# Kernel tuning notes

Measured on AMD Instinct MI355X. Metric: run time of the kernel, lower is better.

## Reference

```python
import jax, jax.numpy as jnp
import numpy as np

N, IN_FEATS, HIDDEN, N_CLASSES = 12000, 256, 256, 40
EPS = 1e-12  # F.normalize default eps


def setup_inputs() -> dict:
    key = jax.random.key(0)
    ks = jax.random.split(key, 6)
    # dense adjacency, scaled like a row-normalized graph operator
    adj = jax.random.uniform(ks[0], (N, N), jnp.float32) * (1.0 / 64.0)
    x = jax.random.normal(ks[1], (N, IN_FEATS), jnp.float32)
    # xavier-uniform-like weights, zero biases (matches init_params)
    def xavier(k, fan_in, fan_out):
        lim = np.sqrt(6.0 / (fan_in + fan_out)).astype(np.float32)
        return jax.random.uniform(k, (fan_in, fan_out), jnp.float32, -lim, lim)
    W0 = xavier(ks[2], IN_FEATS, HIDDEN)
    W1 = xavier(ks[3], HIDDEN, HIDDEN)
    W2 = xavier(ks[4], HIDDEN, N_CLASSES)
    b0 = jnp.zeros((HIDDEN,), jnp.float32)
    b1 = jnp.zeros((HIDDEN,), jnp.float32)
    b2 = jnp.zeros((N_CLASSES,), jnp.float32)
    return {"adj": adj, "x": x, "W0": W0, "b0": b0, "W1": W1, "b1": b1, "W2": W2, "b2": b2}


def _l2_normalize(h):
    # F.normalize(h): rows divided by max(||row||_2, eps)
    norm = jnp.sqrt(jnp.sum(h * h, axis=1, keepdims=True))
    return h / jnp.maximum(norm, EPS)


def reference(adj, x, W0, b0, W1, b1, W2, b2):
    # layer 0: aggregate -> linear -> bias -> relu -> l2-normalize (dropout=eval identity)
    h = _l2_normalize(jax.nn.relu((adj @ x) @ W0 + b0))
    # layer 1 (hidden)
    h = _l2_normalize(jax.nn.relu((adj @ h) @ W1 + b1))
    # output layer: no activation / normalize / dropout
    h = (adj @ h) @ W2 + b2
    return h
```

## Files before the change

kernel.cpp:

```cpp
#include <hip/hip_runtime.h>
#include <hip/hip_bf16.h>

#define M_ROWS 12000
#define K_PAD  12032
#define FEAT   256
#define NCLS   40
#define NSLICE 5
#define NTILES 188
#define NBM    47
#define PSLABE (M_ROWS * FEAT)
#define TILE_SHORTS 16384
#define HALF_SHORTS 8192
#define ITILE 16384
#define IHALF 8192

typedef __attribute__((ext_vector_type(4))) float f32x4;
typedef __attribute__((ext_vector_type(8))) short s16x8;
typedef __attribute__((ext_vector_type(4))) short s16x4;
typedef __attribute__((ext_vector_type(4))) int   i32x4;
typedef __attribute__((ext_vector_type(2))) int   i32x2;
typedef unsigned int u32;

__device__ __forceinline__ short f2bf(float f){
  __hip_bfloat16 h = __float2bfloat16(f);
  union { __hip_bfloat16 h; short s; } u; u.h = h; return u.s;
}
__device__ __forceinline__ float bf2f(short s){
  union { float f; u32 u; } v; v.u = ((u32)(unsigned short)s) << 16; return v.f;
}

__device__ __forceinline__ f32x4 mfma16(s16x8 a, s16x8 b, f32x4 c){
  return __builtin_amdgcn_mfma_f32_16x16x32_bf16(a, b, c, 0, 0, 0);
}

__device__ __forceinline__ void gl16(const void* g, void* l){
  __builtin_amdgcn_global_load_lds(
      (const __attribute__((address_space(1))) u32*)g,
      (__attribute__((address_space(3))) u32*)l, 16, 0, 0);
}

#define VM6   do { asm volatile("s_waitcnt vmcnt(6)" ::: "memory"); \
                   __builtin_amdgcn_sched_barrier(0); } while(0)
#define VM4   do { asm volatile("s_waitcnt vmcnt(4)" ::: "memory"); \
                   __builtin_amdgcn_sched_barrier(0); } while(0)
#define VM2   do { asm volatile("s_waitcnt vmcnt(2)" ::: "memory"); \
                   __builtin_amdgcn_sched_barrier(0); } while(0)
#define VM0   do { asm volatile("s_waitcnt vmcnt(0)" ::: "memory"); \
                   __builtin_amdgcn_sched_barrier(0); } while(0)
#define LGK0  do { asm volatile("s_waitcnt lgkmcnt(0)" ::: "memory"); \
                   __builtin_amdgcn_sched_barrier(0); } while(0)
#define BARR  do { __builtin_amdgcn_s_barrier(); \
                   __builtin_amdgcn_sched_barrier(0); } while(0)

__device__ __forceinline__ int swz(int r){ return (r & 3) ^ ((r >> 2) & 3); }

__device__ __forceinline__ int q8(float v, float s){ return (int)(v * s + 0.5f); }

__global__ __launch_bounds__(256) void k_transpose_pack(const float* __restrict__ src,
                                                        short* __restrict__ Bpack){
  const int t = threadIdx.x;
  if (blockIdx.x == 375){
    short* d = Bpack + (size_t)187 * TILE_SHORTS + HALF_SHORTS + t * 32;
    s16x8 z = (s16x8)0;
    #pragma unroll
    for (int i = 0; i < 4; ++i) *(s16x8*)(d + 8*i) = z;
    return;
  }
  __shared__ float tile[32][257];
  const int r0 = blockIdx.x * 32;
  {
    const int r = t >> 3, cs = (t & 7) * 32;
    const float* s = src + (size_t)(r0 + r) * FEAT + cs;
    #pragma unroll
    for (int i = 0; i < 8; ++i){
      f32x4 v = *(const f32x4*)(s + 4*i);
      tile[r][cs + 4*i + 0] = v[0];
      tile[r][cs + 4*i + 1] = v[1];
      tile[r][cs + 4*i + 2] = v[2];
      tile[r][cs + 4*i + 3] = v[3];
    }
  }
  __syncthreads();
  const int c = t;
  const int kt = r0 >> 6, hh = (r0 >> 5) & 1, sc = swz(c);
  short* d = Bpack + (size_t)kt * TILE_SHORTS + hh * HALF_SHORTS + c * 32;
  #pragma unroll
  for (int i = 0; i < 4; ++i){
    s16x8 o;
    #pragma unroll
    for (int j = 0; j < 8; ++j) o[j] = f2bf(tile[8*i + j][c]);
    *(s16x8*)(d + ((i ^ sc) * 8)) = o;
  }
}

__global__ __launch_bounds__(256) void k_zpad(char* __restrict__ Bpk8){
  const int t = threadIdx.x;
  i32x4 z = {0,0,0,0};
  *(i32x4*)(Bpk8 + (size_t)187 * ITILE + IHALF + t * 16) = z;
  *(i32x4*)(Bpk8 + (size_t)187 * ITILE + IHALF + 4096 + t * 16) = z;
}

__global__ __launch_bounds__(512, 2) void k_gemm_l0(const float* __restrict__ adj,
                                                    const short* __restrict__ Bpack,
                                                    char* __restrict__ Apk8,
                                                    short* __restrict__ Pbase){
  __shared__ __align__(16) short lds[2][4][8192];

  const int t = threadIdx.x;
  const int w = t >> 6, l = t & 63;
  const int wm = w >> 2, wn = w & 3;
  const int lr = l & 15, lg = l >> 4;

  int id = blockIdx.x;
  {
    const int xcd = id & 7, idx = id >> 3;
    id = (xcd < 3 ? xcd * 30 : 90 + (xcd - 3) * 29) + idx;
  }
  const int bm = id % NBM, s = id / NBM;
  const int row0 = bm * 256;
  const int u0  = (s < 3) ? s * 38 : 114 + (s - 3) * 37;
  const int nst = (s < 3) ? 38 : 37;

  const char* Bb = (const char*)Bpack;
  const size_t tp = (size_t)t * 16;
  char* Aw = Apk8 + (size_t)bm * NTILES * ITILE;

  size_t abase[2];
  #pragma unroll
  for (int p = 0; p < 2; ++p){
    const int si = p * 512 + t;
    const int r  = si >> 2, sl = si & 3;
    int grow = row0 + r; if (grow > M_ROWS - 1) grow = M_ROWS - 1;
    abase[p] = (size_t)grow * M_ROWS + (size_t)((sl ^ swz(r)) * 8);
  }

  f32x4 av0[4], av1[4];

#define ISSUE_A0(kt) do{ \
    av0[0] = *(const f32x4*)(adj + abase[0] + (kt)*64);      \
    av0[1] = *(const f32x4*)(adj + abase[0] + (kt)*64 + 4);  \
    av0[2] = *(const f32x4*)(adj + abase[1] + (kt)*64);      \
    av0[3] = *(const f32x4*)(adj + abase[1] + (kt)*64 + 4); }while(0)
#define ISSUE_A1(kt) do{ \
    av1[0] = *(const f32x4*)(adj + abase[0] + (kt)*64 + 32);     \
    av1[1] = *(const f32x4*)(adj + abase[0] + (kt)*64 + 32 + 4); \
    av1[2] = *(const f32x4*)(adj + abase[1] + (kt)*64 + 32);     \
    av1[3] = *(const f32x4*)(adj + abase[1] + (kt)*64 + 32 + 4); }while(0)

#define CVT_WRITE_A(q, h, kt, AV) do{                                         \
    _Pragma("unroll")                                                         \
    for (int p = 0; p < 2; ++p){                                              \
      s16x8 o;                                                                \
      _Pragma("unroll")                                                       \
      for (int j = 0; j < 4; ++j){ o[j] = f2bf(AV[2*p][j]); o[4+j] = f2bf(AV[2*p+1][j]); } \
      const int si = p * 512 + t;                                             \
      *(s16x8*)&lds[q][h][si * 8] = o;                                        \
      int w0_ = 0, w1_ = 0;                                                   \
      _Pragma("unroll")                                                       \
      for (int j = 0; j < 4; ++j){                                            \
        w0_ |= (q8(AV[2*p][j],   8128.0f) & 255) << (8*j);                    \
        w1_ |= (q8(AV[2*p+1][j], 8128.0f) & 255) << (8*j);                    \
      }                                                                       \
      i32x2 pk_; pk_[0] = w0_; pk_[1] = w1_;                                  \
      *(i32x2*)(Aw + (size_t)(kt) * ITILE + (h) * IHALF + si * 8) = pk_;      \
    } }while(0)

#define ST_BH(q, h, kt) do{                                                   \
    const char* s_ = Bb + (size_t)(kt) * 32768 + (h) * 16384 + tp;            \
    gl16(s_,        (char*)&lds[q][2+(h)][0] + w*1024);                       \
    gl16(s_ + 8192, (char*)&lds[q][2+(h)][0] + 8192 + w*1024); }while(0)

#define AF(q, h, mf) \
    (*(const s16x8*)&lds[q][h][ (wm*128 + (mf)*16 + lr) * 32 + \
      ((lg ^ swz(wm*128 + (mf)*16 + lr)) * 8) ])
#define BF(q, h, nf) \
    (*(const s16x8*)&lds[q][2+(h)][ (wn*64 + (nf)*16 + lr) * 32 + \
      ((lg ^ swz(wn*64 + (nf)*16 + lr)) * 8) ])

  f32x4 acc[8][4];
  #pragma unroll
  for (int m = 0; m < 8; ++m)
    #pragma unroll
    for (int n = 0; n < 4; ++n) acc[m][n] = (f32x4)(0.0f);

  ISSUE_A0(u0); ST_BH(0, 0, u0);
  ISSUE_A1(u0); ST_BH(0, 1, u0);
  VM6;  CVT_WRITE_A(0, 0, u0, av0);
  VM4;  CVT_WRITE_A(0, 1, u0, av1);
  LGK0;
  BARR;

  for (int t2 = 0; t2 < nst; ++t2){
    const int q = t2 & 1, qn = q ^ 1;
    const bool stg = (t2 + 1 < nst);
    const int ktn = u0 + t2 + 1;

    s16x8 bfr[4], af[4];

    #pragma unroll
    for (int n = 0; n < 4; ++n) bfr[n] = BF(q, 0, n);
    #pragma unroll
    for (int m = 0; m < 4; ++m) af[m] = AF(q, 0, m);
    if (stg){ ISSUE_A0(ktn); ST_BH(qn, 0, ktn); }
    BARR;
    __builtin_amdgcn_s_setprio(1);
    #pragma unroll
    for (int m = 0; m < 4; ++m)
      #pragma unroll
      for (int n = 0; n < 4; ++n)
        acc[m][n] = mfma16(af[m], bfr[n], acc[m][n]);
    __builtin_amdgcn_s_setprio(0);
    BARR;

    #pragma unroll
    for (int m = 0; m < 4; ++m) af[m] = AF(q, 0, m + 4);
    if (stg){ ISSUE_A1(ktn); ST_BH(qn, 1, ktn); }
    BARR;
    __builtin_amdgcn_s_setprio(1);
    #pragma unroll
    for (int m = 0; m < 4; ++m)
      #pragma unroll
      for (int n = 0; n < 4; ++n)
        acc[m + 4][n] = mfma16(af[m], bfr[n], acc[m + 4][n]);
    __builtin_amdgcn_s_setprio(0);
    BARR;

    if (stg) { VM6; } else { VM4; }
    #pragma unroll
    for (int n = 0; n < 4; ++n) bfr[n] = BF(q, 1, n);
    #pragma unroll
    for (int m = 0; m < 4; ++m) af[m] = AF(q, 1, m);
    if (stg){ CVT_WRITE_A(qn, 0, ktn, av0); }
    BARR;
    __builtin_amdgcn_s_setprio(1);
    #pragma unroll
    for (int m = 0; m < 4; ++m)
      #pragma unroll
      for (int n = 0; n < 4; ++n)
        acc[m][n] = mfma16(af[m], bfr[n], acc[m][n]);
    __builtin_amdgcn_s_setprio(0);
    BARR;

    #pragma unroll
    for (int m = 0; m < 4; ++m) af[m] = AF(q, 1, m + 4);
    if (stg){ VM4; CVT_WRITE_A(qn, 1, ktn, av1); }
    BARR;
    __builtin_amdgcn_s_setprio(1);
    #pragma unroll
    for (int m = 0; m < 4; ++m)
      #pragma unroll
      for (int n = 0; n < 4; ++n)
        acc[m + 4][n] = mfma16(af[m], bfr[n], acc[m + 4][n]);
    __builtin_amdgcn_s_setprio(0);
    if (stg) LGK0;
    BARR;
  }
#undef ISSUE_A0
#undef ISSUE_A1
#undef CVT_WRITE_A
#undef ST_BH
#undef AF
#undef BF

  short* P = Pbase + (size_t)s * PSLABE;
  #pragma unroll
  for (int m = 0; m < 8; ++m){
    const int row = row0 + wm*128 + m*16 + lg*4;
    #pragma unroll
    for (int n = 0; n < 4; ++n){
      const int col = wn*64 + n*16 + lr;
      short* pp = P + (size_t)row * FEAT + col;
      #pragma unroll
      for (int r = 0; r < 4; ++r)
        if (row + r < M_ROWS) pp[(size_t)r * FEAT] = f2bf(acc[m][n][r]);
    }
  }
}

__global__ __launch_bounds__(512, 2) void k_gemm8i(const char* __restrict__ Apk8,
                                                   const char* __restrict__ Bpk8,
                                                   short* __restrict__ Pbase){
  __shared__ __align__(16) char lds8[2][4][8192];

  const int t = threadIdx.x;
  const int w = t >> 6, l = t & 63;
  const int wm = w >> 2, wn = w & 3;
  const int lr = l & 15, lg = l >> 4;

  int id = blockIdx.x;
  {
    const int xcd = id & 7, idx = id >> 3;
    id = (xcd < 3 ? xcd * 30 : 90 + (xcd - 3) * 29) + idx;
  }
  const int bm = id % NBM, s = id / NBM;
  const int row0 = bm * 256;
  const int u0  = (s < 3) ? s * 38 : 114 + (s - 3) * 37;
  const int nst = (s < 3) ? 38 : 37;

  const char* Ab = Apk8 + (size_t)bm * NTILES * ITILE;
  const char* Bb = Bpk8;
  const size_t tp = (size_t)t * 16;

#define ST_AH(q, h, kt) \
    gl16(Ab + (size_t)(kt) * ITILE + (h) * IHALF + tp, (char*)&lds8[q][h][0] + w*1024)
#define ST_BH(q, h, kt) \
    gl16(Bb + (size_t)(kt) * ITILE + (h) * IHALF + tp, (char*)&lds8[q][2+(h)][0] + w*1024)

#define AF8(q, h, mf) \
    (*(const long*)&lds8[q][h][ (wm*128 + (mf)*16 + lr) * 32 + \
      ((lg ^ swz(wm*128 + (mf)*16 + lr)) * 8) ])
#define BF8(q, h, nf) \
    (*(const long*)&lds8[q][2+(h)][ (wn*64 + (nf)*16 + lr) * 32 + \
      ((lg ^ swz(wn*64 + (nf)*16 + lr)) * 8) ])

  i32x4 acc[8][4];
  #pragma unroll
  for (int m = 0; m < 8; ++m)
    #pragma unroll
    for (int n = 0; n < 4; ++n) acc[m][n] = (i32x4){0,0,0,0};

  ST_BH(0, 0, u0); ST_AH(0, 0, u0);
  ST_BH(0, 1, u0); ST_AH(0, 1, u0);
  VM2;
  BARR;

  for (int t2 = 0; t2 < nst; ++t2){
    const int q = t2 & 1, qn = q ^ 1;
    const bool stg = (t2 + 1 < nst);
    const int ktn = u0 + t2 + 1;

    long bfr[4], af[4];

    #pragma unroll
    for (int n = 0; n < 4; ++n) bfr[n] = BF8(q, 0, n);
    #pragma unroll
    for (int m = 0; m < 4; ++m) af[m] = AF8(q, 0, m);
    if (stg) ST_BH(qn, 0, ktn);
    BARR;
    __builtin_amdgcn_s_setprio(1);
    #pragma unroll
    for (int m = 0; m < 4; ++m)
      #pragma unroll
      for (int n = 0; n < 4; ++n)
        acc[m][n] = __builtin_amdgcn_mfma_i32_16x16x32_i8(af[m], bfr[n], acc[m][n], 0, 0, 0);
    __builtin_amdgcn_s_setprio(0);
    BARR;

    #pragma unroll
    for (int m = 0; m < 4; ++m) af[m] = AF8(q, 0, m + 4);
    if (stg) ST_AH(qn, 0, ktn);
    BARR;
    __builtin_amdgcn_s_setprio(1);
    #pragma unroll
    for (int m = 0; m < 4; ++m)
      #pragma unroll
      for (int n = 0; n < 4; ++n)
        acc[m + 4][n] = __builtin_amdgcn_mfma_i32_16x16x32_i8(af[m], bfr[n], acc[m + 4][n], 0, 0, 0);
    __builtin_amdgcn_s_setprio(0);
    if (stg) { VM2; } else { VM0; }
    BARR;

    #pragma unroll
    for (int n = 0; n < 4; ++n) bfr[n] = BF8(q, 1, n);
    #pragma unroll
    for (int m = 0; m < 4; ++m) af[m] = AF8(q, 1, m);
    if (stg) ST_BH(qn, 1, ktn);
    BARR;
    __builtin_amdgcn_s_setprio(1);
    #pragma unroll
    for (int m = 0; m < 4; ++m)
      #pragma unroll
      for (int n = 0; n < 4; ++n)
        acc[m][n] = __builtin_amdgcn_mfma_i32_16x16x32_i8(af[m], bfr[n], acc[m][n], 0, 0, 0);
    __builtin_amdgcn_s_setprio(0);
    BARR;

    #pragma unroll
    for (int m = 0; m < 4; ++m) af[m] = AF8(q, 1, m + 4);
    if (stg) ST_AH(qn, 1, ktn);
    BARR;
    __builtin_amdgcn_s_setprio(1);
    #pragma unroll
    for (int m = 0; m < 4; ++m)
      #pragma unroll
      for (int n = 0; n < 4; ++n)
        acc[m + 4][n] = __builtin_amdgcn_mfma_i32_16x16x32_i8(af[m], bfr[n], acc[m + 4][n], 0, 0, 0);
    __builtin_amdgcn_s_setprio(0);
    if (stg) { VM2; }
    BARR;
  }
#undef ST_AH
#undef ST_BH
#undef AF8
#undef BF8

  const float ds = 1.0f / 1032256.0f;
  short* P = Pbase + (size_t)s * PSLABE;
  #pragma unroll
  for (int m = 0; m < 8; ++m){
    const int row = row0 + wm*128 + m*16 + lg*4;
    #pragma unroll
    for (int n = 0; n < 4; ++n){
      const int col = wn*64 + n*16 + lr;
      short* pp = P + (size_t)row * FEAT + col;
      #pragma unroll
      for (int r = 0; r < 4; ++r)
        if (row + r < M_ROWS) pp[(size_t)r * FEAT] = f2bf((float)acc[m][n][r] * ds);
    }
  }
}

__global__ __launch_bounds__(256) void k_fused2(const short* __restrict__ Pb,
                                                const float* __restrict__ W,
                                                const float* __restrict__ b,
                                                char* __restrict__ Bpk8){
  __shared__ float ylds[32][257];
  __shared__ float red[32][33];
  __shared__ float scale[32];
  const int t  = threadIdx.x;
  const int r0 = blockIdx.x * 32;
  {
    const int r = t >> 3, cs = (t & 7) * 32;
    const size_t off = (size_t)(r0 + r) * FEAT + cs;
    float aa[32];
    {
      const short* p0 = Pb + off;
      #pragma unroll
      for (int i4 = 0; i4 < 4; ++i4){
        s16x8 v = *(const s16x8*)(p0 + i4*8);
        #pragma unroll
        for (int e = 0; e < 8; ++e) aa[i4*8 + e] = bf2f(v[e]);
      }
    }
    #pragma unroll
    for (int s = 1; s < NSLICE; ++s){
      const short* ps = Pb + (size_t)s * PSLABE + off;
      #pragma unroll
      for (int i4 = 0; i4 < 4; ++i4){
        s16x8 v = *(const s16x8*)(ps + i4*8);
        #pragma unroll
        for (int e = 0; e < 8; ++e) aa[i4*8 + e] += bf2f(v[e]);
      }
    }
    #pragma unroll
    for (int k = 0; k < 32; ++k) ylds[r][cs + k] = aa[k];
  }
  __syncthreads();

  const int rg = t >> 5;
  const int cg = t & 31;
  float acc[4][8];
  {
    float bias[8];
    #pragma unroll
    for (int j = 0; j < 8; ++j) bias[j] = b[cg*8 + j];
    #pragma unroll
    for (int i = 0; i < 4; ++i)
      #pragma unroll
      for (int j = 0; j < 8; ++j) acc[i][j] = bias[j];
  }

  #pragma unroll 4
  for (int k = 0; k < FEAT; ++k){
    float yv[4];
    #pragma unroll
    for (int i = 0; i < 4; ++i) yv[i] = ylds[rg*4 + i][k];
    f32x4 w0 = *(const f32x4*)(W + (size_t)k * FEAT + cg*8);
    f32x4 w1 = *(const f32x4*)(W + (size_t)k * FEAT + cg*8 + 4);
    #pragma unroll
    for (int i = 0; i < 4; ++i){
      #pragma unroll
      for (int j = 0; j < 4; ++j){
        acc[i][j]     += yv[i] * w0[j];
        acc[i][4 + j] += yv[i] * w1[j];
      }
    }
  }

  #pragma unroll
  for (int i = 0; i < 4; ++i){
    float ss = 0.0f;
    #pragma unroll
    for (int j = 0; j < 8; ++j){
      float v = fmaxf(acc[i][j], 0.0f);
      acc[i][j] = v;
      ss += v * v;
    }
    red[rg*4 + i][cg] = ss;
  }
  __syncthreads();
  if (t < 32){
    float ssum = 0.0f;
    #pragma unroll
    for (int j = 0; j < 32; ++j) ssum += red[t][j];
    scale[t] = 1.0f / fmaxf(sqrtf(ssum), 1e-12f);
  }
  __syncthreads();

  float sc[4];
  float dith[4];
  #pragma unroll
  for (int i = 0; i < 4; ++i){
    sc[i] = scale[rg*4 + i];
    const int k = r0 + rg*4 + i;
    float x = (float)k * 0.6180339887f;
    dith[i] = x - floorf(x);
  }

  const int kb = r0 + rg * 4;
  const int kt = kb >> 6, hh = (kb >> 5) & 1, g = (kb >> 3) & 3, e0 = kb & 7;
  char* dbase = Bpk8 + (size_t)kt * ITILE + hh * IHALF;
  #pragma unroll
  for (int j = 0; j < 8; ++j){
    const int c = cg * 8 + j;
    int pk = 0;
    #pragma unroll
    for (int i = 0; i < 4; ++i){
      int q = (int)(acc[i][j] * sc[i] * 127.0f + dith[i]);
      pk |= (q & 255) << (8*i);
    }
    *(int*)(dbase + c * 32 + ((g ^ swz(c)) * 8) + e0) = pk;
  }
}

__global__ __launch_bounds__(256) void k_final2(const short* __restrict__ Pb,
                                                const float* __restrict__ W2,
                                                const float* __restrict__ b2,
                                                float* __restrict__ out){
  __shared__ float ylds[32][257];
  const int t  = threadIdx.x;
  const int r0 = blockIdx.x * 32;
  {
    const int r = t >> 3, cs = (t & 7) * 32;
    const size_t off = (size_t)(r0 + r) * FEAT + cs;
    float aa[32];
    {
      const short* p0 = Pb + off;
      #pragma unroll
      for (int i4 = 0; i4 < 4; ++i4){
        s16x8 v = *(const s16x8*)(p0 + i4*8);
        #pragma unroll
        for (int e = 0; e < 8; ++e) aa[i4*8 + e] = bf2f(v[e]);
      }
    }
    #pragma unroll
    for (int s = 1; s < NSLICE; ++s){
      const short* ps = Pb + (size_t)s * PSLABE + off;
      #pragma unroll
      for (int i4 = 0; i4 < 4; ++i4){
        s16x8 v = *(const s16x8*)(ps + i4*8);
        #pragma unroll
        for (int e = 0; e < 8; ++e) aa[i4*8 + e] += bf2f(v[e]);
      }
    }
    #pragma unroll
    for (int k = 0; k < 32; ++k) ylds[r][cs + k] = aa[k];
  }
  __syncthreads();

  #pragma unroll
  for (int e = t; e < 32 * NCLS; e += 256){
    const int r = e / NCLS, n = e % NCLS;
    float a = b2[n];
    #pragma unroll 8
    for (int k = 0; k < FEAT; ++k)
      a = fmaf(ylds[r][k], W2[(size_t)k * NCLS + n], a);
    out[(size_t)(r0 + r) * NCLS + n] = a;
  }
}

extern "C" void kernel_launch(void* const* d_in, const int* in_sizes, int n_in,
                              void* d_out, int out_size, void* d_ws, size_t ws_size,
                              hipStream_t stream){
  const float* adj = (const float*)d_in[0];
  const float* x   = (const float*)d_in[1];
  const float* W0  = (const float*)d_in[2];
  const float* b0  = (const float*)d_in[3];
  const float* W1  = (const float*)d_in[4];
  const float* b1  = (const float*)d_in[5];
  const float* W2  = (const float*)d_in[6];
  const float* b2  = (const float*)d_in[7];
  float* out = (float*)d_out;

  char* ws = (char*)d_ws;
  const size_t BPACK_BYTES = (size_t)NTILES * TILE_SHORTS * 2;
  const size_t BPK8_BYTES  = (size_t)NTILES * ITILE;
  const size_t APK8_BYTES  = (size_t)NBM * NTILES * ITILE;

  short* Bpack = (short*)ws;
  char*  Bpk8  = ws + BPACK_BYTES;
  char*  Apk8  = ws + BPACK_BYTES + BPK8_BYTES;
  short* P     = (short*)(ws + BPACK_BYTES + BPK8_BYTES + APK8_BYTES);

  const dim3 b256(256), b512(512);

  k_transpose_pack<<<376, b256, 0, stream>>>(x, Bpack);
  k_zpad<<<1, b256, 0, stream>>>(Bpk8);

  k_gemm_l0<<<NBM * NSLICE, b512, 0, stream>>>(adj, Bpack, Apk8, P);
  k_fused2<<<375, b256, 0, stream>>>(P, W0, b0, Bpk8);
  k_gemm8i<<<NBM * NSLICE, b512, 0, stream>>>(Apk8, Bpk8, P);
  k_fused2<<<375, b256, 0, stream>>>(P, W1, b1, Bpk8);
  k_gemm8i<<<NBM * NSLICE, b512, 0, stream>>>(Apk8, Bpk8, P);
  k_final2<<<375, b256, 0, stream>>>(P, W2, b2, out);
}
```

Before: 433.5 us.

## Split adjacency int8 quantization into a separate pass; layer-0 GEMM reads int8

```diff
diff --git a/kernel.cpp b/kernel.cpp
--- a/kernel.cpp
+++ b/kernel.cpp
@@ -18,7 +18,6 @@
 typedef __attribute__((ext_vector_type(8))) short s16x8;
 typedef __attribute__((ext_vector_type(4))) short s16x4;
 typedef __attribute__((ext_vector_type(4))) int   i32x4;
-typedef __attribute__((ext_vector_type(2))) int   i32x2;
 typedef unsigned int u32;
 
 __device__ __forceinline__ short f2bf(float f){
@@ -39,10 +38,6 @@
       (__attribute__((address_space(3))) u32*)l, 16, 0, 0);
 }
 
-#define VM6   do { asm volatile("s_waitcnt vmcnt(6)" ::: "memory"); \
-                   __builtin_amdgcn_sched_barrier(0); } while(0)
-#define VM4   do { asm volatile("s_waitcnt vmcnt(4)" ::: "memory"); \
-                   __builtin_amdgcn_sched_barrier(0); } while(0)
 #define VM2   do { asm volatile("s_waitcnt vmcnt(2)" ::: "memory"); \
                    __builtin_amdgcn_sched_barrier(0); } while(0)
 #define VM0   do { asm volatile("s_waitcnt vmcnt(0)" ::: "memory"); \
@@ -100,11 +95,57 @@
   *(i32x4*)(Bpk8 + (size_t)187 * ITILE + IHALF + 4096 + t * 16) = z;
 }
 
-__global__ __launch_bounds__(512, 2) void k_gemm_l0(const float* __restrict__ adj,
-                                                    const short* __restrict__ Bpack,
-                                                    char* __restrict__ Apk8,
-                                                    short* __restrict__ Pbase){
-  __shared__ __align__(16) short lds[2][4][8192];
+__global__ __launch_bounds__(512) void k_conv8(const float* __restrict__ adj,
+                                               char* __restrict__ Apk8){
+  __shared__ char stg[8][12352];
+  const int t  = threadIdx.x;
+  const int rb = blockIdx.x * 8;
+  const int bm = rb >> 8;
+  const int rbase_loc = rb & 255;
+
+  for (int r = 0; r < 8; ++r){
+    const int R = rb + r;
+    const float* rowp = adj + (size_t)(R < M_ROWS ? R : 0) * M_ROWS;
+    #pragma unroll
+    for (int ch = 0; ch < 6; ++ch){
+      const int c0 = ch * 2048 + t * 4;
+      f32x4 v = (f32x4)(0.0f);
+      if (R < M_ROWS && c0 < M_ROWS) v = *(const f32x4*)(rowp + c0);
+      int pk = 0;
+      #pragma unroll
+      for (int j = 0; j < 4; ++j) pk |= (q8(v[j], 8128.0f) & 255) << (8*j);
+      *(int*)&stg[r][c0] = pk;
+    }
+  }
+  __syncthreads();
+
+  char* out = Apk8 + (size_t)bm * NTILES * ITILE;
+  #pragma unroll
+  for (int it = 0; it < 12; ++it){
+    const int tau = t + it * 512;
+    if (tau < 6016){
+      const int p = tau >> 4, c = tau & 15;
+      const int tl = p >> 1, h = p & 1;
+      const int r = c >> 1, sl2 = (c & 1) * 2;
+      const int rloc = rbase_loc + r;
+      const int sw = swz(rloc);
+      const int colb = tl * 64 + h * 32;
+      long lo = *(const long*)&stg[r][colb + ((sl2     ^ sw) * 8)];
+      long hi = *(const long*)&stg[r][colb + (((sl2+1) ^ sw) * 8)];
+      i32x4 o;
+      o[0] = (int)lo; o[1] = (int)(lo >> 32);
+      o[2] = (int)hi; o[3] = (int)(hi >> 32);
+      *(i32x4*)(out + (size_t)tl * ITILE + h * IHALF + rloc * 32 + sl2 * 8) = o;
+    }
+  }
+}
+
+__global__ __launch_bounds__(512, 2) void k_gemm_l0b(const char* __restrict__ Apk8,
+                                                     const short* __restrict__ Bpack,
+                                                     short* __restrict__ Pbase){
+  __shared__ __align__(16) short Abf[2][2][8192];
+  __shared__ __align__(16) short Bl [2][2][8192];
+  __shared__ __align__(16) char  Ai8[16384];
 
   const int t = threadIdx.x;
   const int w = t >> 6, l = t & 63;
@@ -121,60 +162,40 @@
   const int u0  = (s < 3) ? s * 38 : 114 + (s - 3) * 37;
   const int nst = (s < 3) ? 38 : 37;
 
-  const char* Bb = (const char*)Bpack;
+  const char* Ab8 = Apk8 + (size_t)bm * NTILES * ITILE;
+  const char* Bb  = (const char*)Bpack;
   const size_t tp = (size_t)t * 16;
-  char* Aw = Apk8 + (size_t)bm * NTILES * ITILE;
-
-  size_t abase[2];
-  #pragma unroll
-  for (int p = 0; p < 2; ++p){
-    const int si = p * 512 + t;
-    const int r  = si >> 2, sl = si & 3;
-    int grow = row0 + r; if (grow > M_ROWS - 1) grow = M_ROWS - 1;
-    abase[p] = (size_t)grow * M_ROWS + (size_t)((sl ^ swz(r)) * 8);
-  }
-
-  f32x4 av0[4], av1[4];
-
-#define ISSUE_A0(kt) do{ \
-    av0[0] = *(const f32x4*)(adj + abase[0] + (kt)*64);      \
-    av0[1] = *(const f32x4*)(adj + abase[0] + (kt)*64 + 4);  \
-    av0[2] = *(const f32x4*)(adj + abase[1] + (kt)*64);      \
-    av0[3] = *(const f32x4*)(adj + abase[1] + (kt)*64 + 4); }while(0)
-#define ISSUE_A1(kt) do{ \
-    av1[0] = *(const f32x4*)(adj + abase[0] + (kt)*64 + 32);     \
-    av1[1] = *(const f32x4*)(adj + abase[0] + (kt)*64 + 32 + 4); \
-    av1[2] = *(const f32x4*)(adj + abase[1] + (kt)*64 + 32);     \
-    av1[3] = *(const f32x4*)(adj + abase[1] + (kt)*64 + 32 + 4); }while(0)
-
-#define CVT_WRITE_A(q, h, kt, AV) do{                                         \
+
+#define ST_B(q, h, kt) do{                                                    \
+    const char* s_ = Bb + (size_t)(kt) * 32768 + (h) * 16384 + tp;            \
+    gl16(s_,        (char*)&Bl[q][h][0] + w*1024);                            \
+    gl16(s_ + 8192, (char*)&Bl[q][h][0] + 8192 + w*1024); }while(0)
+#define ST_AI(kt) do{                                                         \
+    gl16(Ab8 + (size_t)(kt) * ITILE + tp,        (char*)Ai8 + w*1024);        \
+    gl16(Ab8 + (size_t)(kt) * ITILE + 8192 + tp, (char*)Ai8 + 8192 + w*1024); }while(0)
+
+#define CONV_A(qn) do{                                                        \
+    const int h_ = t >> 8;                                                    \
+    const int ti = (t & 255) * 32;                                            \
+    const char* sp = &Ai8[h_*8192 + ti];                                      \
+    short* dp = &Abf[qn][h_][ti];                                             \
     _Pragma("unroll")                                                         \
-    for (int p = 0; p < 2; ++p){                                              \
+    for (int j = 0; j < 4; ++j){                                              \
+      long v = *(const long*)(sp + j*8);                                      \
       s16x8 o;                                                                \
       _Pragma("unroll")                                                       \
-      for (int j = 0; j < 4; ++j){ o[j] = f2bf(AV[2*p][j]); o[4+j] = f2bf(AV[2*p+1][j]); } \
-      const int si = p * 512 + t;                                             \
-      *(s16x8*)&lds[q][h][si * 8] = o;                                        \
-      int w0_ = 0, w1_ = 0;                                                   \
-      _Pragma("unroll")                                                       \
-      for (int j = 0; j < 4; ++j){                                            \
-        w0_ |= (q8(AV[2*p][j],   8128.0f) & 255) << (8*j);                    \
-        w1_ |= (q8(AV[2*p+1][j], 8128.0f) & 255) << (8*j);                    \
+      for (int e = 0; e < 8; ++e){                                            \
+        int b_ = (int)((unsigned long)(v >> (8*e)) & 255);                    \
+        o[e] = f2bf((float)b_ * (1.0f/8128.0f));                              \
       }                                                                       \
-      i32x2 pk_; pk_[0] = w0_; pk_[1] = w1_;                                  \
-      *(i32x2*)(Aw + (size_t)(kt) * ITILE + (h) * IHALF + si * 8) = pk_;      \
+      *(s16x8*)(dp + j*8) = o;                                                \
     } }while(0)
 
-#define ST_BH(q, h, kt) do{                                                   \
-    const char* s_ = Bb + (size_t)(kt) * 32768 + (h) * 16384 + tp;            \
-    gl16(s_,        (char*)&lds[q][2+(h)][0] + w*1024);                       \
-    gl16(s_ + 8192, (char*)&lds[q][2+(h)][0] + 8192 + w*1024); }while(0)
-
-#define AF(q, h, mf) \
-    (*(const s16x8*)&lds[q][h][ (wm*128 + (mf)*16 + lr) * 32 + \
+#define AFb(q, h, mf) \
+    (*(const s16x8*)&Abf[q][h][ (wm*128 + (mf)*16 + lr) * 32 + \
       ((lg ^ swz(wm*128 + (mf)*16 + lr)) * 8) ])
-#define BF(q, h, nf) \
-    (*(const s16x8*)&lds[q][2+(h)][ (wn*64 + (nf)*16 + lr) * 32 + \
+#define BFb(q, h, nf) \
+    (*(const s16x8*)&Bl[q][h][ (wn*64 + (nf)*16 + lr) * 32 + \
       ((lg ^ swz(wn*64 + (nf)*16 + lr)) * 8) ])
 
   f32x4 acc[8][4];
@@ -183,11 +204,11 @@
     #pragma unroll
     for (int n = 0; n < 4; ++n) acc[m][n] = (f32x4)(0.0f);
 
-  ISSUE_A0(u0); ST_BH(0, 0, u0);
-  ISSUE_A1(u0); ST_BH(0, 1, u0);
-  VM6;  CVT_WRITE_A(0, 0, u0, av0);
-  VM4;  CVT_WRITE_A(0, 1, u0, av1);
-  LGK0;
+  ST_B(0, 0, u0); ST_AI(u0); ST_B(0, 1, u0);
+  VM2;
+  BARR;
+  CONV_A(0);
+  VM0; LGK0;
   BARR;
 
   for (int t2 = 0; t2 < nst; ++t2){
@@ -198,10 +219,10 @@
     s16x8 bfr[4], af[4];
 
     #pragma unroll
-    for (int n = 0; n < 4; ++n) bfr[n] = BF(q, 0, n);
-    #pragma unroll
-    for (int m = 0; m < 4; ++m) af[m] = AF(q, 0, m);
-    if (stg){ ISSUE_A0(ktn); ST_BH(qn, 0, ktn); }
+    for (int n = 0; n < 4; ++n) bfr[n] = BFb(q, 0, n);
+    #pragma unroll
+    for (int m = 0; m < 4; ++m) af[m] = AFb(q, 0, m);
+    if (stg){ ST_B(qn, 0, ktn); ST_AI(ktn); }
     BARR;
     __builtin_amdgcn_s_setprio(1);
     #pragma unroll
@@ -213,8 +234,8 @@
     BARR;
 
     #pragma unroll
-    for (int m = 0; m < 4; ++m) af[m] = AF(q, 0, m + 4);
-    if (stg){ ISSUE_A1(ktn); ST_BH(qn, 1, ktn); }
+    for (int m = 0; m < 4; ++m) af[m] = AFb(q, 0, m + 4);
+    if (stg) ST_B(qn, 1, ktn);
     BARR;
     __builtin_amdgcn_s_setprio(1);
     #pragma unroll
@@ -225,12 +246,10 @@
     __builtin_amdgcn_s_setprio(0);
     BARR;
 
-    if (stg) { VM6; } else { VM4; }
-    #pragma unroll
-    for (int n = 0; n < 4; ++n) bfr[n] = BF(q, 1, n);
-    #pragma unroll
-    for (int m = 0; m < 4; ++m) af[m] = AF(q, 1, m);
-    if (stg){ CVT_WRITE_A(qn, 0, ktn, av0); }
+    #pragma unroll
+    for (int n = 0; n < 4; ++n) bfr[n] = BFb(q, 1, n);
+    #pragma unroll
+    for (int m = 0; m < 4; ++m) af[m] = AFb(q, 1, m);
     BARR;
     __builtin_amdgcn_s_setprio(1);
     #pragma unroll
@@ -242,9 +261,10 @@
     BARR;
 
     #pragma unroll
-    for (int m = 0; m < 4; ++m) af[m] = AF(q, 1, m + 4);
-    if (stg){ VM4; CVT_WRITE_A(qn, 1, ktn, av1); }
-    BARR;
+    for (int m = 0; m < 4; ++m) af[m] = AFb(q, 1, m + 4);
+    if (stg) { VM2; }
+    BARR;
+    if (stg) { CONV_A(qn); }
     __builtin_amdgcn_s_setprio(1);
     #pragma unroll
     for (int m = 0; m < 4; ++m)
@@ -252,15 +272,14 @@
       for (int n = 0; n < 4; ++n)
         acc[m + 4][n] = mfma16(af[m], bfr[n], acc[m + 4][n]);
     __builtin_amdgcn_s_setprio(0);
-    if (stg) LGK0;
-    BARR;
-  }
-#undef ISSUE_A0
-#undef ISSUE_A1
-#undef CVT_WRITE_A
-#undef ST_BH
-#undef AF
-#undef BF
+    if (stg){ VM0; LGK0; }
+    BARR;
+  }
+#undef ST_B
+#undef ST_AI
+#undef CONV_A
+#undef AFb
+#undef BFb
 
   short* P = Pbase + (size_t)s * PSLABE;
   #pragma unroll
@@ -596,8 +615,9 @@
 
   k_transpose_pack<<<376, b256, 0, stream>>>(x, Bpack);
   k_zpad<<<1, b256, 0, stream>>>(Bpk8);
-
-  k_gemm_l0<<<NBM * NSLICE, b512, 0, stream>>>(adj, Bpack, Apk8, P);
+  k_conv8<<<1504, b512, 0, stream>>>(adj, Apk8);
+
+  k_gemm_l0b<<<NBM * NSLICE, b512, 0, stream>>>(Apk8, Bpack, P);
   k_fused2<<<375, b256, 0, stream>>>(P, W0, b0, Bpk8);
   k_gemm8i<<<NBM * NSLICE, b512, 0, stream>>>(Apk8, Bpk8, P);
   k_fused2<<<375, b256, 0, stream>>>(P, W1, b1, Bpk8);
```

After: 554.1 us. 27.8% more time.
